# Performance work log

Measured on AMD Instinct MI355X. Metric: run time of the kernel, lower is better.

## Reference

```python
import jax, jax.numpy as jnp
import numpy as np


def setup_inputs() -> dict:
    key = jax.random.key(0)
    k1, k2, k3 = jax.random.split(key, 3)
    B, C, H, W = 16, 32, 48, 48
    inp = jax.random.normal(k1, (B, C, H, W), dtype=jnp.float32)
    # weight channels encode a CxC matrix per pixel; add identity (in the
    # flattened C*C channel layout) so every per-pixel matrix is well
    # conditioned for solve/slogdet, as a trained flow's weights would be.
    w = jax.random.normal(k2, (B, C * C, H, W), dtype=jnp.float32) * 0.1
    eye = jnp.eye(C, dtype=jnp.float32).reshape(C * C, 1, 1)
    w = w + eye
    logdet = jax.random.normal(k3, (B,), dtype=jnp.float32)
    return {"input": inp, "weight": w, "logdet": logdet}


def reference(input, weight, logdet):
    # forward (reverse=False) path of InvConditionalLinear
    B, C, H, W = input.shape
    # [B, C*C, H, W] -> [B, H, W, C, C] per-pixel matrices
    w = jnp.transpose(weight, (0, 2, 3, 1)).reshape(B, H, W, C, C)
    # sum of per-pixel log|det W| over all pixels -> [B]
    weight_logdet = jnp.sum(jnp.linalg.slogdet(w)[1], axis=(1, 2))
    # batched per-pixel solve: W z = x
    rhs = jnp.transpose(input, (0, 2, 3, 1))[..., None]  # [B,H,W,C,1]
    z = jnp.linalg.solve(w, rhs)[..., 0]                  # [B,H,W,C]
    z = jnp.transpose(z, (0, 3, 1, 2))                    # [B,C,H,W]
    return z, logdet - weight_logdet
```

## Files before the change

### kernel.cpp

```cpp
#include <hip/hip_runtime.h>
#include <math.h>

#define CDIM 32
#define HWDIM 2304
#define BDIM 16
#define PPW 8
#define NTHREADS 256
#define PPB 32
#define ZOFF (BDIM * CDIM * HWDIM)

__device__ __forceinline__ void gload_lds16(const float* g, float* l) {
    __builtin_amdgcn_global_load_lds(
        (const __attribute__((address_space(1))) float*)g,
        (__attribute__((address_space(3))) float*)l, 16, 0, 0);
}

__global__ __launch_bounds__(NTHREADS, 2)
void solve_kernel(const float* __restrict__ input,
                  const float* __restrict__ weight,
                  const float* __restrict__ logdet,
                  float* __restrict__ out) {
    const int t    = threadIdx.x;
    const int lane = t & 63;
    const int wv   = t >> 6;
    const int h    = lane & 7;
    const int p    = lane >> 3;
    const int gb   = lane & 56;

    const int blk  = blockIdx.x;
    const int b    = blk / (HWDIM / PPB);
    const int pb   = (blk % (HWDIM / PPB)) * PPB;
    const int pixl = wv * PPW + p;
    const int pix0 = pb + wv * PPW;
    const int pix  = pb + pixl;

    __shared__ float lds[2][256 * CDIM];

    const float* xp = input + (size_t)b * CDIM * HWDIM + (size_t)h * HWDIM + pix;
    float y[4];
    #pragma unroll
    for (int r = 0; r < 4; ++r) y[r] = xp[(size_t)(r * 8) * HWDIM];
    asm volatile("" ::: "memory");

    const int sg = lane >> 3;
    const int sp = lane & 7;
    const int ps = pixl >> 2, pc = pixl & 3;
    const float* wbase = weight + (size_t)b * (CDIM * CDIM) * HWDIM + pb;
    const float* srcA = wbase + (size_t)(wv * 64 + sg) * HWDIM
                              + ((sp ^ (2 * wv)) << 2);
    const float* srcB = wbase + (size_t)(wv * 64 + sg) * HWDIM
                              + ((sp ^ (2 * wv + 1)) << 2);

    auto stage = [&](int r, int buf) {
        float* lbase = &lds[buf][(wv * 64) * CDIM];
        #pragma unroll
        for (int q = 0; q < 8; ++q) {
            const float* s = (q < 4 ? srcA : srcB)
                           + (size_t)(r * 256 + q * 8) * HWDIM;
            gload_lds16(s, lbase + q * 8 * CDIM);
        }
    };

    stage(0, 0);
    asm volatile("" ::: "memory");
    stage(1, 1);

    float A[4][CDIM];
    #pragma unroll
    for (int r = 0; r < 4; ++r) {
        if (r < 3) asm volatile("s_waitcnt vmcnt(8)" ::: "memory");
        else       asm volatile("s_waitcnt vmcnt(0)" ::: "memory");
        __builtin_amdgcn_s_barrier();
        asm volatile("" ::: "memory");
        #pragma unroll
        for (int j = 0; j < CDIM; ++j)
            A[r][j] = lds[r & 1][(h * CDIM + j) * CDIM + ((ps ^ h) << 2) + pc];
        if (r < 2) {
            asm volatile("s_waitcnt lgkmcnt(0)" ::: "memory");
            __builtin_amdgcn_s_barrier();
            asm volatile("" ::: "memory");
            stage(r + 2, r & 1);
        }
    }

    float lacc = 0.0f;
    #pragma unroll
    for (int k = 0; k < CDIM; ++k) {
        const int tr = k >> 3, k7 = k & 7;
        const int src = gb + k7;
        float bp = __shfl(A[tr][k], src);
        float r  = __builtin_amdgcn_rcpf(bp);
        lacc += __log2f(fabsf(bp));

        float m[4];
        m[tr] = (h > k7) ? A[tr][k] * r : ((h == k7) ? (1.0f - r) : 0.0f);
        #pragma unroll
        for (int q = tr + 1; q < 4; ++q) m[q] = A[q][k] * r;

        #pragma unroll
        for (int j = k + 1; j < CDIM; ++j) {
            float bv = __shfl(A[tr][j], src);
            #pragma unroll
            for (int q = tr; q < 4; ++q)
                A[q][j] = fmaf(-m[q], bv, A[q][j]);
        }
        float bq = __shfl(y[tr], src);
        #pragma unroll
        for (int q = tr; q < 4; ++q) y[q] = fmaf(-m[q], bq, y[q]);
    }

    #pragma unroll
    for (int k = CDIM - 1; k >= 1; --k) {
        const int tr = k >> 3, k7 = k & 7;
        const int src = gb + k7;
        float bz = __shfl(y[tr], src);
        float c = (h < k7) ? A[tr][k] : 0.0f;
        y[tr] = fmaf(-c, bz, y[tr]);
        #pragma unroll
        for (int q = 0; q < tr; ++q)
            y[q] = fmaf(-A[q][k], bz, y[q]);
    }

    float* zp = out + (size_t)b * CDIM * HWDIM + (size_t)h * HWDIM + pix;
    #pragma unroll
    for (int r = 0; r < 4; ++r) zp[(size_t)(r * 8) * HWDIM] = y[r];

    float v2 = lacc;
    v2 += __shfl_xor(v2, 8);
    v2 += __shfl_xor(v2, 16);
    v2 += __shfl_xor(v2, 32);
    if (lane == 0) {
        float add = -v2 * 0.69314718055994531f;
        if (pix0 == 0) add += logdet[b];
        atomicAdd(&out[ZOFF + b], add);
    }
}

extern "C" void kernel_launch(void* const* d_in, const int* in_sizes, int n_in,
                              void* d_out, int out_size, void* d_ws, size_t ws_size,
                              hipStream_t stream) {
    const float* input  = (const float*)d_in[0];
    const float* weight = (const float*)d_in[1];
    const float* logdet = (const float*)d_in[2];
    float* out = (float*)d_out;

    solve_kernel<<<BDIM * (HWDIM / PPB), NTHREADS, 0, stream>>>(input, weight,
                                                                logdet, out);
}
```

Before: 258.8 us.

## Replace ds_bpermute shuffles with DPP broadcasts and process two pixel tiles per block

```diff
diff --git a/kernel.cpp b/kernel.cpp
--- a/kernel.cpp
+++ b/kernel.cpp
@@ -7,12 +7,36 @@
 #define PPW 8
 #define NTHREADS 256
 #define PPB 32
+#define BATCH 2
 #define ZOFF (BDIM * CDIM * HWDIM)
 
 __device__ __forceinline__ void gload_lds16(const float* g, float* l) {
     __builtin_amdgcn_global_load_lds(
         (const __attribute__((address_space(1))) float*)g,
         (__attribute__((address_space(3))) float*)l, 16, 0, 0);
+}
+
+__device__ __forceinline__ float bcast8(float x, int k7) {
+    int v = __float_as_int(x), b;
+    switch (k7) {
+    case 0: b = __builtin_amdgcn_update_dpp(v, v, 0x00, 0xF, 0xF, false);
+            b = __builtin_amdgcn_update_dpp(b, b, 0x114, 0xF, 0xA, false); break;
+    case 1: b = __builtin_amdgcn_update_dpp(v, v, 0x55, 0xF, 0xF, false);
+            b = __builtin_amdgcn_update_dpp(b, b, 0x114, 0xF, 0xA, false); break;
+    case 2: b = __builtin_amdgcn_update_dpp(v, v, 0xAA, 0xF, 0xF, false);
+            b = __builtin_amdgcn_update_dpp(b, b, 0x114, 0xF, 0xA, false); break;
+    case 3: b = __builtin_amdgcn_update_dpp(v, v, 0xFF, 0xF, 0xF, false);
+            b = __builtin_amdgcn_update_dpp(b, b, 0x114, 0xF, 0xA, false); break;
+    case 4: b = __builtin_amdgcn_update_dpp(v, v, 0x00, 0xF, 0xF, false);
+            b = __builtin_amdgcn_update_dpp(b, b, 0x104, 0xF, 0x5, false); break;
+    case 5: b = __builtin_amdgcn_update_dpp(v, v, 0x55, 0xF, 0xF, false);
+            b = __builtin_amdgcn_update_dpp(b, b, 0x104, 0xF, 0x5, false); break;
+    case 6: b = __builtin_amdgcn_update_dpp(v, v, 0xAA, 0xF, 0xF, false);
+            b = __builtin_amdgcn_update_dpp(b, b, 0x104, 0xF, 0x5, false); break;
+    default: b = __builtin_amdgcn_update_dpp(v, v, 0xFF, 0xF, 0xF, false);
+            b = __builtin_amdgcn_update_dpp(b, b, 0x104, 0xF, 0x5, false); break;
+    }
+    return __int_as_float(b);
 }
 
 __global__ __launch_bounds__(NTHREADS, 2)
@@ -25,114 +49,123 @@
     const int wv   = t >> 6;
     const int h    = lane & 7;
     const int p    = lane >> 3;
-    const int gb   = lane & 56;
 
     const int blk  = blockIdx.x;
-    const int b    = blk / (HWDIM / PPB);
-    const int pb   = (blk % (HWDIM / PPB)) * PPB;
+    const int BPI  = HWDIM / (PPB * BATCH);
+    const int b    = blk / BPI;
+    const int pbB  = (blk % BPI) * (PPB * BATCH);
     const int pixl = wv * PPW + p;
-    const int pix0 = pb + wv * PPW;
-    const int pix  = pb + pixl;
 
     __shared__ float lds[2][256 * CDIM];
-
-    const float* xp = input + (size_t)b * CDIM * HWDIM + (size_t)h * HWDIM + pix;
-    float y[4];
-    #pragma unroll
-    for (int r = 0; r < 4; ++r) y[r] = xp[(size_t)(r * 8) * HWDIM];
-    asm volatile("" ::: "memory");
 
     const int sg = lane >> 3;
     const int sp = lane & 7;
     const int ps = pixl >> 2, pc = pixl & 3;
-    const float* wbase = weight + (size_t)b * (CDIM * CDIM) * HWDIM + pb;
-    const float* srcA = wbase + (size_t)(wv * 64 + sg) * HWDIM
-                              + ((sp ^ (2 * wv)) << 2);
-    const float* srcB = wbase + (size_t)(wv * 64 + sg) * HWDIM
-                              + ((sp ^ (2 * wv + 1)) << 2);
 
-    auto stage = [&](int r, int buf) {
-        float* lbase = &lds[buf][(wv * 64) * CDIM];
+    #pragma unroll 1
+    for (int bt = 0; bt < BATCH; ++bt) {
+        const int pbt  = pbB + bt * PPB;
+        const int pix  = pbt + pixl;
+        const int pix0 = pbt + wv * PPW;
+
+        const float* xp = input + (size_t)b * CDIM * HWDIM
+                                + (size_t)h * HWDIM + pix;
+        float y[4];
         #pragma unroll
-        for (int q = 0; q < 8; ++q) {
-            const float* s = (q < 4 ? srcA : srcB)
-                           + (size_t)(r * 256 + q * 8) * HWDIM;
-            gload_lds16(s, lbase + q * 8 * CDIM);
+        for (int r = 0; r < 4; ++r) y[r] = xp[(size_t)(r * 8) * HWDIM];
+        asm volatile("" ::: "memory");
+
+        const float* wbase = weight + (size_t)b * (CDIM * CDIM) * HWDIM + pbt;
+        const float* srcA = wbase + (size_t)(wv * 64 + sg) * HWDIM
+                                  + ((sp ^ (2 * wv)) << 2);
+        const float* srcB = wbase + (size_t)(wv * 64 + sg) * HWDIM
+                                  + ((sp ^ (2 * wv + 1)) << 2);
+
+        auto stage = [&](int r, int buf) {
+            float* lbase = &lds[buf][(wv * 64) * CDIM];
+            #pragma unroll
+            for (int q = 0; q < 8; ++q) {
+                const float* s = (q < 4 ? srcA : srcB)
+                               + (size_t)(r * 256 + q * 8) * HWDIM;
+                gload_lds16(s, lbase + q * 8 * CDIM);
+            }
+        };
+
+        stage(0, 0);
+        asm volatile("" ::: "memory");
+        stage(1, 1);
+
+        float A[4][CDIM];
+        #pragma unroll
+        for (int r = 0; r < 4; ++r) {
+            if (r < 3) asm volatile("s_waitcnt vmcnt(8)" ::: "memory");
+            else       asm volatile("s_waitcnt vmcnt(0)" ::: "memory");
+            __builtin_amdgcn_s_barrier();
+            asm volatile("" ::: "memory");
+            #pragma unroll
+            for (int j = 0; j < CDIM; ++j)
+                A[r][j] = lds[r & 1][(h * CDIM + j) * CDIM
+                                     + ((ps ^ h) << 2) + pc];
+            if (r < 2) {
+                asm volatile("s_waitcnt lgkmcnt(0)" ::: "memory");
+                __builtin_amdgcn_s_barrier();
+                asm volatile("" ::: "memory");
+                stage(r + 2, r & 1);
+            }
         }
-    };
 
-    stage(0, 0);
-    asm volatile("" ::: "memory");
-    stage(1, 1);
+        float lacc = 0.0f;
+        #pragma unroll
+        for (int k = 0; k < CDIM; ++k) {
+            const int tr = k >> 3, k7 = k & 7;
+            float bp = bcast8(A[tr][k], k7);
+            float r  = __builtin_amdgcn_rcpf(bp);
+            lacc += __log2f(fabsf(bp));
 
-    float A[4][CDIM];
-    #pragma unroll
-    for (int r = 0; r < 4; ++r) {
-        if (r < 3) asm volatile("s_waitcnt vmcnt(8)" ::: "memory");
-        else       asm volatile("s_waitcnt vmcnt(0)" ::: "memory");
+            float m[4];
+            m[tr] = (h > k7) ? A[tr][k] * r : ((h == k7) ? (1.0f - r) : 0.0f);
+            #pragma unroll
+            for (int q = tr + 1; q < 4; ++q) m[q] = A[q][k] * r;
+
+            #pragma unroll
+            for (int j = k + 1; j < CDIM; ++j) {
+                float bv = bcast8(A[tr][j], k7);
+                #pragma unroll
+                for (int q = tr; q < 4; ++q)
+                    A[q][j] = fmaf(-m[q], bv, A[q][j]);
+            }
+            float bq = bcast8(y[tr], k7);
+            #pragma unroll
+            for (int q = tr; q < 4; ++q) y[q] = fmaf(-m[q], bq, y[q]);
+        }
+
+        #pragma unroll
+        for (int k = CDIM - 1; k >= 1; --k) {
+            const int tr = k >> 3, k7 = k & 7;
+            float bz = bcast8(y[tr], k7);
+            float cm = (h < k7) ? A[tr][k] : 0.0f;
+            y[tr] = fmaf(-cm, bz, y[tr]);
+            #pragma unroll
+            for (int q = 0; q < tr; ++q)
+                y[q] = fmaf(-A[q][k], bz, y[q]);
+        }
+
+        float* zp = out + (size_t)b * CDIM * HWDIM + (size_t)h * HWDIM + pix;
+        #pragma unroll
+        for (int r = 0; r < 4; ++r) zp[(size_t)(r * 8) * HWDIM] = y[r];
+
+        float v2 = lacc;
+        v2 += __shfl_xor(v2, 8);
+        v2 += __shfl_xor(v2, 16);
+        v2 += __shfl_xor(v2, 32);
+        if (lane == 0) {
+            float add = -v2 * 0.69314718055994531f;
+            if (pix0 == 0) add += logdet[b];
+            atomicAdd(&out[ZOFF + b], add);
+        }
+
         __builtin_amdgcn_s_barrier();
         asm volatile("" ::: "memory");
-        #pragma unroll
-        for (int j = 0; j < CDIM; ++j)
-            A[r][j] = lds[r & 1][(h * CDIM + j) * CDIM + ((ps ^ h) << 2) + pc];
-        if (r < 2) {
-            asm volatile("s_waitcnt lgkmcnt(0)" ::: "memory");
-            __builtin_amdgcn_s_barrier();
-            asm volatile("" ::: "memory");
-            stage(r + 2, r & 1);
-        }
-    }
-
-    float lacc = 0.0f;
-    #pragma unroll
-    for (int k = 0; k < CDIM; ++k) {
-        const int tr = k >> 3, k7 = k & 7;
-        const int src = gb + k7;
-        float bp = __shfl(A[tr][k], src);
-        float r  = __builtin_amdgcn_rcpf(bp);
-        lacc += __log2f(fabsf(bp));
-
-        float m[4];
-        m[tr] = (h > k7) ? A[tr][k] * r : ((h == k7) ? (1.0f - r) : 0.0f);
-        #pragma unroll
-        for (int q = tr + 1; q < 4; ++q) m[q] = A[q][k] * r;
-
-        #pragma unroll
-        for (int j = k + 1; j < CDIM; ++j) {
-            float bv = __shfl(A[tr][j], src);
-            #pragma unroll
-            for (int q = tr; q < 4; ++q)
-                A[q][j] = fmaf(-m[q], bv, A[q][j]);
-        }
-        float bq = __shfl(y[tr], src);
-        #pragma unroll
-        for (int q = tr; q < 4; ++q) y[q] = fmaf(-m[q], bq, y[q]);
-    }
-
-    #pragma unroll
-    for (int k = CDIM - 1; k >= 1; --k) {
-        const int tr = k >> 3, k7 = k & 7;
-        const int src = gb + k7;
-        float bz = __shfl(y[tr], src);
-        float c = (h < k7) ? A[tr][k] : 0.0f;
-        y[tr] = fmaf(-c, bz, y[tr]);
-        #pragma unroll
-        for (int q = 0; q < tr; ++q)
-            y[q] = fmaf(-A[q][k], bz, y[q]);
-    }
-
-    float* zp = out + (size_t)b * CDIM * HWDIM + (size_t)h * HWDIM + pix;
-    #pragma unroll
-    for (int r = 0; r < 4; ++r) zp[(size_t)(r * 8) * HWDIM] = y[r];
-
-    float v2 = lacc;
-    v2 += __shfl_xor(v2, 8);
-    v2 += __shfl_xor(v2, 16);
-    v2 += __shfl_xor(v2, 32);
-    if (lane == 0) {
-        float add = -v2 * 0.69314718055994531f;
-        if (pix0 == 0) add += logdet[b];
-        atomicAdd(&out[ZOFF + b], add);
     }
 }
 
@@ -144,6 +177,6 @@
     const float* logdet = (const float*)d_in[2];
     float* out = (float*)d_out;
 
-    solve_kernel<<<BDIM * (HWDIM / PPB), NTHREADS, 0, stream>>>(input, weight,
-                                                                logdet, out);
+    solve_kernel<<<BDIM * (HWDIM / (PPB * BATCH)), NTHREADS, 0, stream>>>(
+        input, weight, logdet, out);
 }
```

Measured after the change: 443.4 us. 71.3% more time.
